# Kernel tuning notes

Hardware: AMD Instinct MI355X
Metric: run time of the kernel (lower is better)

Reference implementation:

```python
import jax, jax.numpy as jnp
import numpy as np

B, S, D = 4, 2048, 1024
H, DK, DV = 16, 64, 64


def setup_inputs() -> dict:
    key = jax.random.key(0)
    ks = jax.random.split(key, 12)
    sd = 1.0 / np.sqrt(D)
    sdo = 1.0 / np.sqrt(DV * H)
    return {
        "query": jax.random.normal(ks[0], (B, S, D), jnp.float32),
        "key": jax.random.normal(ks[1], (B, S, D), jnp.float32),
        "value": jax.random.normal(ks[2], (B, S, D), jnp.float32),
        "mask": jnp.zeros((B, 1, 1, S), jnp.float32),
        "Wq": jax.random.uniform(ks[3], (D, DK * H), jnp.float32, -sd, sd),
        "bq": jax.random.uniform(ks[4], (DK * H,), jnp.float32, -sd, sd),
        "Wk": jax.random.uniform(ks[5], (D, DK * H), jnp.float32, -sd, sd),
        "bk": jax.random.uniform(ks[6], (DK * H,), jnp.float32, -sd, sd),
        "Wv": jax.random.uniform(ks[7], (D, DV * H), jnp.float32, -sd, sd),
        "bv": jax.random.uniform(ks[8], (DV * H,), jnp.float32, -sd, sd),
        "Wo": jax.random.uniform(ks[9], (DV * H, D), jnp.float32, -sdo, sdo),
        "bo": jax.random.uniform(ks[10], (D,), jnp.float32, -sdo, sdo),
    }


def reference(query, key, value, mask, Wq, bq, Wk, bk, Wv, bv, Wo, bo):
    b, sq, _ = query.shape
    # QKV projections -> (B, H, S, d)
    Q = (query @ Wq + bq).reshape(b, sq, H, DK).transpose(0, 2, 1, 3)
    K = (key @ Wk + bk).reshape(b, key.shape[1], H, DK).transpose(0, 2, 1, 3)
    V = (value @ Wv + bv).reshape(b, value.shape[1], H, DV).transpose(0, 2, 1, 3)
    # scaled dot-product attention with additive mask
    scores = jnp.einsum("bhqd,bhkd->bhqk", Q, K) / jnp.sqrt(jnp.float32(DK))
    scores = scores + mask  # mask broadcast over heads/query positions
    probs = jax.nn.softmax(scores, axis=-1)
    # weighted values, merge heads -> (B, S, H*DV)
    weights = jnp.einsum("bhqk,bhkd->bhqd", probs, V).transpose(0, 2, 1, 3).reshape(b, sq, H * DV)
    output = weights @ Wo + bo  # dropout p=0 (eval) -> identity
    return (output, weights)
```

## Files before the change

### kernel.cpp

```cpp
#include <hip/hip_runtime.h>
#include <hip/hip_bf16.h>

typedef __attribute__((ext_vector_type(8))) short bf16x8;
typedef __attribute__((ext_vector_type(8))) short short8v;
typedef __attribute__((ext_vector_type(4))) float f32x4;

__device__ __forceinline__ short f2bf(float x) {
  union { __hip_bfloat16 h; short s; } u;
  u.h = __float2bfloat16(x);
  return u.s;
}

__device__ __forceinline__ void async16(const void* g, void* l) {
  __builtin_amdgcn_global_load_lds(
      (const __attribute__((address_space(1))) unsigned int*)g,
      (__attribute__((address_space(3))) unsigned int*)l, 16, 0, 0);
}

__device__ __forceinline__ void stage8k(const char* gbase, int rowStride, short* lds, int tid) {
  int wave = tid >> 6, lane = tid & 63;
#pragma unroll
  for (int j = 0; j < 2; ++j) {
    int chunk = wave * 128 + j * 64 + lane;
    int row = chunk >> 3;
    int colb = (chunk & 7) << 4;
    const char* src = gbase + row * rowStride + (colb ^ ((row & 7) << 4));
    char* dst = (char*)lds + (wave * 128 + j * 64) * 16;
    async16(src, dst);
  }
}

__global__ __launch_bounds__(256) void cvtw_k(const float* Wq, const float* Wk,
                                              const float* Wv, const float* Wo, short* Wt) {
  int t = blockIdx.x * 256 + threadIdx.x;
  int mat = t >> 18;
  int rem = t & 262143;
  int row = rem >> 8;
  int col4 = rem & 255;
  const float* src = mat == 0 ? Wq : (mat == 1 ? Wk : (mat == 2 ? Wv : Wo));
  float4 v = *(const float4*)(src + (size_t)row * 1024 + col4 * 4);
  short* dstm = Wt + (size_t)mat * 1048576;
  int n = col4 * 4;
  dstm[(size_t)(n + 0) * 1024 + row] = f2bf(v.x);
  dstm[(size_t)(n + 1) * 1024 + row] = f2bf(v.y);
  dstm[(size_t)(n + 2) * 1024 + row] = f2bf(v.z);
  dstm[(size_t)(n + 3) * 1024 + row] = f2bf(v.w);
}

__global__ __launch_bounds__(256) void cvta_k(const float* q, const float* k,
                                              const float* v, short* out) {
  int z = blockIdx.y;
  const float* src = z == 0 ? q : (z == 1 ? k : v);
  size_t base = ((size_t)blockIdx.x * 256 + threadIdx.x) * 8;
  float4 a = *(const float4*)(src + base);
  float4 b2 = *(const float4*)(src + base + 4);
  short8v h;
  h[0] = f2bf(a.x);  h[1] = f2bf(a.y);  h[2] = f2bf(a.z);  h[3] = f2bf(a.w);
  h[4] = f2bf(b2.x); h[5] = f2bf(b2.y); h[6] = f2bf(b2.z); h[7] = f2bf(b2.w);
  *(short8v*)(out + (size_t)z * 8388608 + base) = h;
}

template <int MODE>
__global__ __launch_bounds__(256) void gemm_k(
    const short* Ab, const short* Wt, const float* bias0, const float* bias1,
    short* Qp, short* Kp, short* Vpt, float* outF) {
  __shared__ short As[2][128 * 32];
  __shared__ short Bs[2][128 * 32];
  int tid = threadIdx.x, lane = tid & 63, wave = tid >> 6;
  int g = lane >> 4, c = lane & 15;
  int n0 = blockIdx.x * 128, m0 = blockIdx.y * 128, z = blockIdx.z;

  const short* Az = (MODE == 0) ? Ab + (size_t)z * 8388608 : Ab;
  const short* Wz = (MODE == 0) ? Wt + (size_t)z * 1048576 : Wt;
  const float* bias = (MODE == 0) ? (z == 0 ? bias0 : bias1) : bias0;

  auto stage = [&](int ks, int buf) {
    const char* ga = (const char*)Az + ((size_t)m0 * 1024 + ks * 32) * 2;
    const char* gb = (const char*)Wz + ((size_t)n0 * 1024 + ks * 32) * 2;
#pragma unroll
    for (int i = 0; i < 2; ++i) {
      int ch = i * 256 + tid;
      int row = ch >> 2, slot = ch & 3;
      int sw = ((row >> 1) & 3) << 4;
      char* dstA = (char*)&As[buf][0] + (i * 256 + wave * 64) * 16;
      char* dstB = (char*)&Bs[buf][0] + (i * 256 + wave * 64) * 16;
      async16(ga + (size_t)row * 2048 + ((slot << 4) ^ sw), dstA);
      async16(gb + (size_t)row * 2048 + ((slot << 4) ^ sw), dstB);
    }
  };

  f32x4 acc[4][4];
#pragma unroll
  for (int i = 0; i < 4; ++i)
#pragma unroll
    for (int j = 0; j < 4; ++j) acc[i][j] = (f32x4){0.f, 0.f, 0.f, 0.f};

  int wr = (wave >> 1) * 64, wc = (wave & 1) * 64;

  stage(0, 0);
  for (int ks = 0; ks < 32; ++ks) {
    __syncthreads();
    if (ks + 1 < 32) stage(ks + 1, (ks & 1) ^ 1);
    int cur = ks & 1;
    bf16x8 af[4], bfv[4];
#pragma unroll
    for (int mt = 0; mt < 4; ++mt) {
      int r_ = wr + mt * 16 + c;
      af[mt] = *(const bf16x8*)((const char*)&As[cur][0] + r_ * 64 +
                                ((g << 4) ^ ((((r_ >> 1) & 3)) << 4)));
    }
#pragma unroll
    for (int nt = 0; nt < 4; ++nt) {
      int r_ = wc + nt * 16 + c;
      bfv[nt] = *(const bf16x8*)((const char*)&Bs[cur][0] + r_ * 64 +
                                 ((g << 4) ^ ((((r_ >> 1) & 3)) << 4)));
    }
#pragma unroll
    for (int mt = 0; mt < 4; ++mt)
#pragma unroll
      for (int nt = 0; nt < 4; ++nt) {
        if (MODE == 1)
          acc[mt][nt] = __builtin_amdgcn_mfma_f32_16x16x32_bf16(af[mt], bfv[nt], acc[mt][nt], 0, 0, 0);
        else
          acc[mt][nt] = __builtin_amdgcn_mfma_f32_16x16x32_bf16(bfv[nt], af[mt], acc[mt][nt], 0, 0, 0);
      }
  }

  if (MODE == 0) {
    short* dst0 = (z == 0) ? Qp : Kp;
    float scale = (z == 0) ? 0.125f : 1.f;
#pragma unroll
    for (int nt = 0; nt < 4; ++nt) {
      int nb = n0 + wc + nt * 16 + g * 4;
      float4 b4 = *(const float4*)(bias + nb);
      int d0 = nb & 63, nh = nb >> 6;
#pragma unroll
      for (int mt = 0; mt < 4; ++mt) {
        int m = m0 + wr + mt * 16 + c;
        int bh = (m >> 11) * 16 + nh;
        short4 hv;
        hv.x = f2bf((acc[mt][nt][0] + b4.x) * scale);
        hv.y = f2bf((acc[mt][nt][1] + b4.y) * scale);
        hv.z = f2bf((acc[mt][nt][2] + b4.z) * scale);
        hv.w = f2bf((acc[mt][nt][3] + b4.w) * scale);
        *(short4*)(dst0 + ((size_t)bh * 2048 + (m & 2047)) * 64 + d0) = hv;
      }
    }
  } else if (MODE == 1) {
#pragma unroll
    for (int nt = 0; nt < 4; ++nt) {
      int n = n0 + wc + nt * 16 + c;
      float bb = bias[n];
      int d = n & 63, nh = n >> 6;
#pragma unroll
      for (int mt = 0; mt < 4; ++mt) {
        int mb = m0 + wr + mt * 16 + g * 4;
        int bh = (mb >> 11) * 16 + nh;
        short4 hv;
        hv.x = f2bf(acc[mt][nt][0] + bb);
        hv.y = f2bf(acc[mt][nt][1] + bb);
        hv.z = f2bf(acc[mt][nt][2] + bb);
        hv.w = f2bf(acc[mt][nt][3] + bb);
        *(short4*)(Vpt + ((size_t)bh * 64 + d) * 2048 + (mb & 2047)) = hv;
      }
    }
  } else {
#pragma unroll
    for (int nt = 0; nt < 4; ++nt) {
      int nb = n0 + wc + nt * 16 + g * 4;
      float4 b4 = *(const float4*)(bias + nb);
#pragma unroll
      for (int mt = 0; mt < 4; ++mt) {
        int m = m0 + wr + mt * 16 + c;
        float4 o;
        o.x = acc[mt][nt][0] + b4.x;
        o.y = acc[mt][nt][1] + b4.y;
        o.z = acc[mt][nt][2] + b4.z;
        o.w = acc[mt][nt][3] + b4.w;
        *(float4*)(outF + (size_t)m * 1024 + nb) = o;
      }
    }
  }
}

__global__ __launch_bounds__(256) void attn_k(const short* Qp, const short* Kp,
                                              const short* Vpt, const float* mask,
                                              float* outW, short* wbf) {
  __shared__ short Qs[64 * 64];
  __shared__ short Ks[2][64 * 64];
  __shared__ short Vs[2][64 * 64];
  __shared__ short Ps[64 * 64];
  int tid = threadIdx.x, lane = tid & 63, wave = tid >> 6;
  int g = lane >> 4, c = lane & 15;
  int qt = blockIdx.x, bh = blockIdx.y;
  int b = bh >> 4, h = bh & 15;

  const char* Qg = (const char*)Qp + ((size_t)bh * 2048 + qt * 64) * 128;
  const char* Kg = (const char*)Kp + (size_t)bh * 2048 * 128;
  const char* Vg = (const char*)Vpt + (size_t)bh * 64 * 4096;

  stage8k(Qg, 128, Qs, tid);
  stage8k(Kg, 128, Ks[0], tid);
  stage8k(Vg, 4096, Vs[0], tid);

  f32x4 acco[4];
#pragma unroll
  for (int i = 0; i < 4; ++i) acco[i] = (f32x4){0.f, 0.f, 0.f, 0.f};
  float mrun = -1e30f, lrun = 0.f;

  __syncthreads();

  int qrow = wave * 16 + c;
  bf16x8 aq[2];
#pragma unroll
  for (int k2 = 0; k2 < 2; ++k2)
    aq[k2] = *(const bf16x8*)((const char*)Qs + qrow * 128 +
                              ((k2 * 64 + g * 16) ^ ((qrow & 7) << 4)));

  int cur = 0;
  for (int t = 0; t < 32; ++t) {
    if (t + 1 < 32) {
      stage8k(Kg + (size_t)(t + 1) * 8192, 128, Ks[cur ^ 1], tid);
      stage8k(Vg + (size_t)(t + 1) * 128, 4096, Vs[cur ^ 1], tid);
    }
    f32x4 sc[4];
#pragma unroll
    for (int n = 0; n < 4; ++n) {
      sc[n] = (f32x4){0.f, 0.f, 0.f, 0.f};
#pragma unroll
      for (int k2 = 0; k2 < 2; ++k2) {
        int row = n * 16 + c;
        bf16x8 bk = *(const bf16x8*)((const char*)&Ks[cur][0] + row * 128 +
                                     ((k2 * 64 + g * 16) ^ ((row & 7) << 4)));
        sc[n] = __builtin_amdgcn_mfma_f32_16x16x32_bf16(bk, aq[k2], sc[n], 0, 0, 0);
      }
    }
#pragma unroll
    for (int n = 0; n < 4; ++n) {
      float4 mk = *(const float4*)(mask + (size_t)b * 2048 + t * 64 + n * 16 + g * 4);
      sc[n][0] += mk.x; sc[n][1] += mk.y; sc[n][2] += mk.z; sc[n][3] += mk.w;
    }
    float tmax = sc[0][0];
#pragma unroll
    for (int n = 0; n < 4; ++n)
#pragma unroll
      for (int r = 0; r < 4; ++r) tmax = fmaxf(tmax, sc[n][r]);
    tmax = fmaxf(tmax, __shfl_xor(tmax, 16));
    tmax = fmaxf(tmax, __shfl_xor(tmax, 32));
    if (!__all(tmax <= mrun + 8.0f)) {
      float mnew = fmaxf(mrun, tmax);
      float fsc = __expf(mrun - mnew);
      mrun = mnew;
      lrun *= fsc;
#pragma unroll
      for (int n = 0; n < 4; ++n)
#pragma unroll
        for (int r = 0; r < 4; ++r) acco[n][r] *= fsc;
    }
    float p[4][4], rs = 0.f;
#pragma unroll
    for (int n = 0; n < 4; ++n)
#pragma unroll
      for (int r = 0; r < 4; ++r) {
        p[n][r] = __expf(sc[n][r] - mrun);
        rs += p[n][r];
      }
    rs += __shfl_xor(rs, 16);
    rs += __shfl_xor(rs, 32);
    lrun += rs;
#pragma unroll
    for (int n = 0; n < 4; ++n) {
      short4 hv;
      hv.x = f2bf(p[n][0]); hv.y = f2bf(p[n][1]);
      hv.z = f2bf(p[n][2]); hv.w = f2bf(p[n][3]);
      int colb = (n * 32 + g * 8) ^ ((qrow & 7) << 4);
      *(short4*)((char*)Ps + qrow * 128 + colb) = hv;
    }
#pragma unroll
    for (int k2 = 0; k2 < 2; ++k2) {
      bf16x8 ap = *(const bf16x8*)((const char*)Ps + qrow * 128 +
                                   ((k2 * 64 + g * 16) ^ ((qrow & 7) << 4)));
#pragma unroll
      for (int n2 = 0; n2 < 4; ++n2) {
        int rv = n2 * 16 + c;
        bf16x8 bv = *(const bf16x8*)((const char*)&Vs[cur][0] + rv * 128 +
                                     ((k2 * 64 + g * 16) ^ ((rv & 7) << 4)));
        acco[n2] = __builtin_amdgcn_mfma_f32_16x16x32_bf16(bv, ap, acco[n2], 0, 0, 0);
      }
    }
    __syncthreads();
    cur ^= 1;
  }
  float inv = 1.0f / lrun;
  int srow = qt * 64 + qrow;
#pragma unroll
  for (int n = 0; n < 4; ++n) {
    int col0 = h * 64 + n * 16 + g * 4;
    size_t idx = ((size_t)b * 2048 + srow) * 1024 + col0;
    float4 o;
    o.x = acco[n][0] * inv; o.y = acco[n][1] * inv;
    o.z = acco[n][2] * inv; o.w = acco[n][3] * inv;
    *(float4*)(outW + idx) = o;
    short4 hv;
    hv.x = f2bf(o.x); hv.y = f2bf(o.y); hv.z = f2bf(o.z); hv.w = f2bf(o.w);
    *(short4*)(wbf + idx) = hv;
  }
}

extern "C" void kernel_launch(void* const* d_in, const int* in_sizes, int n_in,
                              void* d_out, int out_size, void* d_ws, size_t ws_size,
                              hipStream_t stream) {
  const float* q    = (const float*)d_in[0];
  const float* k    = (const float*)d_in[1];
  const float* v    = (const float*)d_in[2];
  const float* mask = (const float*)d_in[3];
  const float* Wq   = (const float*)d_in[4];
  const float* bq   = (const float*)d_in[5];
  const float* Wk   = (const float*)d_in[6];
  const float* bk   = (const float*)d_in[7];
  const float* Wv   = (const float*)d_in[8];
  const float* bv   = (const float*)d_in[9];
  const float* Wo   = (const float*)d_in[10];
  const float* bo   = (const float*)d_in[11];

  short* Wt  = (short*)d_ws;
  short* Qp  = Wt + (size_t)4 * 1048576;
  short* Kp  = Qp + (size_t)8388608;
  short* Vpt = Kp + (size_t)8388608;
  short* Wbf = Vpt + (size_t)8388608;

  float* out1 = (float*)d_out;
  float* out2 = out1 + (size_t)8388608;

  short* Abf = (short*)d_out;

  cvtw_k<<<dim3(4096), dim3(256), 0, stream>>>(Wq, Wk, Wv, Wo, Wt);
  cvta_k<<<dim3(4096, 3), dim3(256), 0, stream>>>(q, k, v, Abf);
  gemm_k<0><<<dim3(8, 64, 2), dim3(256), 0, stream>>>(
      Abf, Wt, bq, bk, Qp, Kp, (short*)nullptr, (float*)nullptr);
  gemm_k<1><<<dim3(8, 64, 1), dim3(256), 0, stream>>>(
      Abf + (size_t)2 * 8388608, Wt + (size_t)2 * 1048576, bv, (const float*)nullptr,
      (short*)nullptr, (short*)nullptr, Vpt, (float*)nullptr);
  attn_k<<<dim3(32, 64), dim3(256), 0, stream>>>(Qp, Kp, Vpt, mask, out2, Wbf);
  gemm_k<2><<<dim3(8, 64, 1), dim3(256), 0, stream>>>(
      Wbf, Wt + (size_t)3 * 1048576, bo, (const float*)nullptr,
      (short*)nullptr, (short*)nullptr, (short*)nullptr, out1);
}
```

Baseline: 471.2 us.

## Tighten async-load waits, remap block order, and tile weight transpose through LDS

In the GEMM and attention loops, the full __syncthreads is replaced by explicit vmcnt waits plus raw s_barrier, so the next tile's async global-to-LDS loads can stay in flight while the current tile is computed. MFMA sections are wrapped in s_setprio. Workgroup indices are remapped so neighbouring blocks land on the same XCD for better cache reuse. Attention also prefetches mask values early and reuses the Q LDS buffer for P. The weight conversion kernel now transposes 64x64 tiles through LDS, turning scattered 2-byte stores into coalesced 16-byte stores. The hand-placed waitcnt and barrier logic depends on precise in-flight load counts, so a miscount would cause races.

```diff
diff --git a/kernel.cpp b/kernel.cpp
--- a/kernel.cpp
+++ b/kernel.cpp
@@ -16,6 +16,11 @@
       (const __attribute__((address_space(1))) unsigned int*)g,
       (__attribute__((address_space(3))) unsigned int*)l, 16, 0, 0);
 }
+
+#define VM_WAIT4 do { asm volatile("s_waitcnt vmcnt(4)" ::: "memory"); \
+                      __builtin_amdgcn_sched_barrier(0); } while (0)
+#define VM_WAIT0 do { asm volatile("s_waitcnt vmcnt(0)" ::: "memory"); \
+                      __builtin_amdgcn_sched_barrier(0); } while (0)
 
 __device__ __forceinline__ void stage8k(const char* gbase, int rowStride, short* lds, int tid) {
   int wave = tid >> 6, lane = tid & 63;
@@ -32,19 +37,30 @@
 
 __global__ __launch_bounds__(256) void cvtw_k(const float* Wq, const float* Wk,
                                               const float* Wv, const float* Wo, short* Wt) {
-  int t = blockIdx.x * 256 + threadIdx.x;
-  int mat = t >> 18;
-  int rem = t & 262143;
-  int row = rem >> 8;
-  int col4 = rem & 255;
+  __shared__ short T[64 * 72];
+  int mat = blockIdx.z;
   const float* src = mat == 0 ? Wq : (mat == 1 ? Wk : (mat == 2 ? Wv : Wo));
-  float4 v = *(const float4*)(src + (size_t)row * 1024 + col4 * 4);
+  int n0 = blockIdx.x * 64, k0 = blockIdx.y * 64;
+  int tid = threadIdx.x;
+#pragma unroll
+  for (int i = 0; i < 4; ++i) {
+    int f = i * 256 + tid;
+    int kk = f >> 4, nn4 = (f & 15) * 4;
+    float4 v = *(const float4*)(src + (size_t)(k0 + kk) * 1024 + n0 + nn4);
+    short* d = &T[kk * 72 + nn4];
+    d[0] = f2bf(v.x); d[1] = f2bf(v.y); d[2] = f2bf(v.z); d[3] = f2bf(v.w);
+  }
+  __syncthreads();
   short* dstm = Wt + (size_t)mat * 1048576;
-  int n = col4 * 4;
-  dstm[(size_t)(n + 0) * 1024 + row] = f2bf(v.x);
-  dstm[(size_t)(n + 1) * 1024 + row] = f2bf(v.y);
-  dstm[(size_t)(n + 2) * 1024 + row] = f2bf(v.z);
-  dstm[(size_t)(n + 3) * 1024 + row] = f2bf(v.w);
+#pragma unroll
+  for (int i = 0; i < 2; ++i) {
+    int cidx = i * 256 + tid;
+    int nn = cidx >> 3, kc = (cidx & 7) * 8;
+    short8v o;
+#pragma unroll
+    for (int j = 0; j < 8; ++j) o[j] = T[(kc + j) * 72 + nn];
+    *(short8v*)(dstm + (size_t)(n0 + nn) * 1024 + k0 + kc) = o;
+  }
 }
 
 __global__ __launch_bounds__(256) void cvta_k(const float* q, const float* k,
@@ -68,7 +84,9 @@
   __shared__ short Bs[2][128 * 32];
   int tid = threadIdx.x, lane = tid & 63, wave = tid >> 6;
   int g = lane >> 4, c = lane & 15;
-  int n0 = blockIdx.x * 128, m0 = blockIdx.y * 128, z = blockIdx.z;
+  int orig = blockIdx.x + blockIdx.y * 8;
+  int wg = (orig & 7) * 64 + (orig >> 3);
+  int n0 = (wg & 7) * 128, m0 = (wg >> 3) * 128, z = blockIdx.z;
 
   const short* Az = (MODE == 0) ? Ab + (size_t)z * 8388608 : Ab;
   const short* Wz = (MODE == 0) ? Wt + (size_t)z * 1048576 : Wt;
@@ -99,8 +117,9 @@
 
   stage(0, 0);
   for (int ks = 0; ks < 32; ++ks) {
-    __syncthreads();
-    if (ks + 1 < 32) stage(ks + 1, (ks & 1) ^ 1);
+    if (ks + 1 < 32) { stage(ks + 1, (ks & 1) ^ 1); VM_WAIT4; }
+    else             { VM_WAIT0; }
+    __builtin_amdgcn_s_barrier();
     int cur = ks & 1;
     bf16x8 af[4], bfv[4];
 #pragma unroll
@@ -115,6 +134,7 @@
       bfv[nt] = *(const bf16x8*)((const char*)&Bs[cur][0] + r_ * 64 +
                                  ((g << 4) ^ ((((r_ >> 1) & 3)) << 4)));
     }
+    __builtin_amdgcn_s_setprio(1);
 #pragma unroll
     for (int mt = 0; mt < 4; ++mt)
 #pragma unroll
@@ -124,6 +144,8 @@
         else
           acc[mt][nt] = __builtin_amdgcn_mfma_f32_16x16x32_bf16(bfv[nt], af[mt], acc[mt][nt], 0, 0, 0);
       }
+    __builtin_amdgcn_s_setprio(0);
+    __builtin_amdgcn_s_barrier();
   }
 
   if (MODE == 0) {
@@ -189,10 +211,12 @@
   __shared__ short Qs[64 * 64];
   __shared__ short Ks[2][64 * 64];
   __shared__ short Vs[2][64 * 64];
-  __shared__ short Ps[64 * 64];
+  short* Ps = Qs;
   int tid = threadIdx.x, lane = tid & 63, wave = tid >> 6;
   int g = lane >> 4, c = lane & 15;
-  int qt = blockIdx.x, bh = blockIdx.y;
+  int orig = blockIdx.x + blockIdx.y * 32;
+  int wg = (orig & 7) * 256 + (orig >> 3);
+  int qt = wg & 31, bh = wg >> 5;
   int b = bh >> 4, h = bh & 15;
 
   const char* Qg = (const char*)Qp + ((size_t)bh * 2048 + qt * 64) * 128;
@@ -208,8 +232,7 @@
   for (int i = 0; i < 4; ++i) acco[i] = (f32x4){0.f, 0.f, 0.f, 0.f};
   float mrun = -1e30f, lrun = 0.f;
 
-  __syncthreads();
-
+  VM_WAIT4;
   int qrow = wave * 16 + c;
   bf16x8 aq[2];
 #pragma unroll
@@ -219,11 +242,19 @@
 
   int cur = 0;
   for (int t = 0; t < 32; ++t) {
+    float4 mk[4];
+#pragma unroll
+    for (int n = 0; n < 4; ++n)
+      mk[n] = *(const float4*)(mask + (size_t)b * 2048 + t * 64 + n * 16 + g * 4);
+    __builtin_amdgcn_sched_barrier(0);
     if (t + 1 < 32) {
       stage8k(Kg + (size_t)(t + 1) * 8192, 128, Ks[cur ^ 1], tid);
       stage8k(Vg + (size_t)(t + 1) * 128, 4096, Vs[cur ^ 1], tid);
     }
+    VM_WAIT4;
+    __builtin_amdgcn_s_barrier();
     f32x4 sc[4];
+    __builtin_amdgcn_s_setprio(1);
 #pragma unroll
     for (int n = 0; n < 4; ++n) {
       sc[n] = (f32x4){0.f, 0.f, 0.f, 0.f};
@@ -235,10 +266,11 @@
         sc[n] = __builtin_amdgcn_mfma_f32_16x16x32_bf16(bk, aq[k2], sc[n], 0, 0, 0);
       }
     }
+    __builtin_amdgcn_s_setprio(0);
 #pragma unroll
     for (int n = 0; n < 4; ++n) {
-      float4 mk = *(const float4*)(mask + (size_t)b * 2048 + t * 64 + n * 16 + g * 4);
-      sc[n][0] += mk.x; sc[n][1] += mk.y; sc[n][2] += mk.z; sc[n][3] += mk.w;
+      sc[n][0] += mk[n].x; sc[n][1] += mk[n].y;
+      sc[n][2] += mk[n].z; sc[n][3] += mk[n].w;
     }
     float tmax = sc[0][0];
 #pragma unroll
@@ -276,6 +308,7 @@
       int colb = (n * 32 + g * 8) ^ ((qrow & 7) << 4);
       *(short4*)((char*)Ps + qrow * 128 + colb) = hv;
     }
+    __builtin_amdgcn_s_setprio(1);
 #pragma unroll
     for (int k2 = 0; k2 < 2; ++k2) {
       bf16x8 ap = *(const bf16x8*)((const char*)Ps + qrow * 128 +
@@ -288,7 +321,8 @@
         acco[n2] = __builtin_amdgcn_mfma_f32_16x16x32_bf16(bv, ap, acco[n2], 0, 0, 0);
       }
     }
-    __syncthreads();
+    __builtin_amdgcn_s_setprio(0);
+    __builtin_amdgcn_s_barrier();
     cur ^= 1;
   }
   float inv = 1.0f / lrun;
@@ -334,7 +368,7 @@
 
   short* Abf = (short*)d_out;
 
-  cvtw_k<<<dim3(4096), dim3(256), 0, stream>>>(Wq, Wk, Wv, Wo, Wt);
+  cvtw_k<<<dim3(16, 16, 4), dim3(256), 0, stream>>>(Wq, Wk, Wv, Wo, Wt);
   cvta_k<<<dim3(4096, 3), dim3(256), 0, stream>>>(q, k, v, Abf);
   gemm_k<0><<<dim3(8, 64, 2), dim3(256), 0, stream>>>(
       Abf, Wt, bq, bk, Qp, Kp, (short*)nullptr, (float*)nullptr);
```

Result: faster. 426.1 us (-9.6%).
